# Performance work log

Measured on AMD Instinct MI355X. Metric: run time of the kernel, lower is better.

Reference implementation:

```python
import jax, jax.numpy as jnp
import numpy as np

TOP_K = 2
LORA_SCALE = 32.0 / 16.0  # alpha / r


def setup_inputs() -> dict:
    key = jax.random.key(0)
    ks = jax.random.split(key, 11)
    B, S, H, I, E, R = 4, 2048, 2048, 5504, 8, 16
    s = lambda k, shape, fan: jax.random.normal(k, shape, jnp.float32) / np.sqrt(fan)
    return {
        "x": jax.random.normal(ks[0], (B, S, H), jnp.float32),
        "gate_values": jax.random.normal(ks[1], (B, E), jnp.float32),
        "Wg": s(ks[2], (I, H), H),
        "Ag": s(ks[3], (E, H, R), H),
        "Bg": s(ks[4], (E, R, I), R),
        "Wu": s(ks[5], (I, H), H),
        "Au": s(ks[6], (E, H, R), H),
        "Bu": s(ks[7], (E, R, I), R),
        "Wd": s(ks[8], (H, I), I),
        "Ad": s(ks[9], (E, I, R), I),
        "Bd": s(ks[10], (E, R, H), R),
    }


def _top_k_binary_gates(gate_values, k):
    # set top-k entries per row to 1.0, others 0.0 (bsz, num_experts)
    _, idx = jax.lax.top_k(gate_values, k)
    b = jnp.zeros_like(gate_values)
    rows = jnp.arange(gate_values.shape[0])[:, None]
    return b.at[rows, idx].set(1.0)


def _adapter_linear(x, W, A, B, binary_gates):
    # base: (b,s,in) @ (out,in)^T -> (b,s,out)
    base = jnp.einsum("bsh,oh->bso", x, W)
    # per-expert LoRA: gate e * x @ A_e @ B_e, summed over selected experts
    u = jnp.einsum("bsh,ehr->bser", x, A)            # (b,s,E,r) low-rank
    delta = jnp.einsum("bser,ero,be->bso", u, B, binary_gates)
    return base + LORA_SCALE * delta


def reference(x, gate_values, Wg, Ag, Bg, Wu, Au, Bu, Wd, Ad, Bd):
    g = _top_k_binary_gates(gate_values, TOP_K)
    gate_out = _adapter_linear(x, Wg, Ag, Bg, g)
    up_out = _adapter_linear(x, Wu, Au, Bu, g)
    h = jax.nn.silu(gate_out) * up_out              # SwiGLU
    return _adapter_linear(h, Wd, Ad, Bd, g)
```

## Files before the change

### kernel.cpp

```cpp
#include <hip/hip_runtime.h>
#include <stdint.h>

typedef unsigned short u16;
typedef __bf16 bf16x8 __attribute__((ext_vector_type(8)));
typedef float f32x4 __attribute__((ext_vector_type(4)));

#define AS1 __attribute__((address_space(1)))
#define AS3 __attribute__((address_space(3)))

__device__ __forceinline__ void g2l16(const void* g, void* l) {
  __builtin_amdgcn_global_load_lds((AS1 void*)(void*)g, (AS3 void*)l, 16, 0, 0);
}

__device__ __forceinline__ u16 f2bf(float f) {
  union { float f; uint32_t u; } v; v.f = f;
  return (u16)((v.u + 0x7fffu + ((v.u >> 16) & 1u)) >> 16);
}
__device__ __forceinline__ float bf2f(u16 b) {
  union { uint32_t u; float f; } v; v.u = ((uint32_t)b) << 16;
  return v.f;
}

__global__ void k_top2(const float* __restrict__ gv, int* __restrict__ idx) {
  int b = threadIdx.x;
  if (b < 4) {
    const float* g = gv + b * 8;
    int i1 = 0; float v1 = g[0];
    for (int e = 1; e < 8; ++e) if (g[e] > v1) { v1 = g[e]; i1 = e; }
    int i2 = -1; float v2 = -3.0e38f;
    for (int e = 0; e < 8; ++e) if (e != i1 && g[e] > v2) { v2 = g[e]; i2 = e; }
    idx[2 * b] = i1; idx[2 * b + 1] = i2;
  }
}

__global__ void k_cast(const float* __restrict__ in, u16* __restrict__ out, int n4) {
  int i = blockIdx.x * 256 + threadIdx.x;
  if (i < n4) {
    float4 v = ((const float4*)in)[i];
    ushort4 o = make_ushort4(f2bf(v.x), f2bf(v.y), f2bf(v.z), f2bf(v.w));
    ((ushort4*)out)[i] = o;
  }
}

__global__ void k_aT(const float* __restrict__ A0, const float* __restrict__ A1,
                     const int* __restrict__ idx, u16* __restrict__ out,
                     int Kd, int jmax) {
  int t = blockIdx.x * 256 + threadIdx.x;
  if (t >= 4 * jmax * Kd) return;
  int h = t % Kd;
  int j = (t / Kd) % jmax;
  int b = t / (Kd * jmax);
  const float* src = (j >= 32) ? A1 : A0;
  int jj = j & 31;
  int e = idx[2 * b + ((jj >> 4) & 1)];
  int r = jj & 15;
  out[t] = f2bf(src[((size_t)e * Kd + h) * 16 + r]);
}

__global__ void k_bT(const float* __restrict__ Bsrc, const int* __restrict__ idx,
                     u16* __restrict__ out, int N) {
  int t = blockIdx.x * 256 + threadIdx.x;
  if (t < 4 * N * 32) {
    int j = t & 31;
    int n = (t >> 5) % N;
    int b = t / (N * 32);
    int e = (j & 16) ? idx[2 * b + 1] : idx[2 * b];
    int r = j & 15;
    out[t] = f2bf(Bsrc[((size_t)e * 16 + r) * N + n]);
  }
}

template <int N2>
__global__ __launch_bounds__(256) void k_skinny(
    const u16* __restrict__ A, const u16* __restrict__ BT,
    float* __restrict__ part, int M, int K, int total_iters, int iters_per_chunk) {
  __shared__ u16 sA[128 * 64];
  __shared__ u16 sB[N2 * 64];
  int nm = M >> 7;
  int bm = blockIdx.x % nm, chunk = blockIdx.x / nm;
  int m0 = bm << 7;
  int batch = m0 >> 11;
  int tid = threadIdx.x, lane = tid & 63, w = tid >> 6;
  int kb = chunk * iters_per_chunk;
  int ke = min(total_iters, kb + iters_per_chunk);

  const u16* Bb = BT + (size_t)batch * N2 * K;

  const u16* ga[4]; u16* la[4];
  #pragma unroll
  for (int t = 0; t < 4; ++t) {
    int cb = 4 * w + t;
    int q = cb * 64 + lane;
    int row = q >> 3;
    int c = (q & 7) ^ (row & 7);
    ga[t] = A + (size_t)(m0 + row) * K + (size_t)kb * 64 + c * 8;
    la[t] = sA + cb * 512;
  }
  constexpr int nB = N2 / 32;
  const u16* gb[nB]; u16* lb[nB];
  #pragma unroll
  for (int t = 0; t < nB; ++t) {
    int cb = nB * w + t;
    int q = cb * 64 + lane;
    int row = q >> 3;
    int c = (q & 7) ^ (row & 7);
    gb[t] = Bb + (size_t)row * K + (size_t)kb * 64 + c * 8;
    lb[t] = sB + cb * 512;
  }

  f32x4 acc[2][N2 / 16] = {};
  for (int kt = kb; kt < ke; ++kt) {
    #pragma unroll
    for (int t = 0; t < 4; ++t) { g2l16(ga[t], la[t]); ga[t] += 64; }
    #pragma unroll
    for (int t = 0; t < nB; ++t) { g2l16(gb[t], lb[t]); gb[t] += 64; }
    __syncthreads();
    #pragma unroll
    for (int ks = 0; ks < 2; ++ks) {
      int cb0 = ks * 4 + (lane >> 4);
      bf16x8 af[2], bfr[N2 / 16];
      #pragma unroll
      for (int mi = 0; mi < 2; ++mi) {
        int row = 32 * w + mi * 16 + (lane & 15);
        af[mi] = *(const bf16x8*)(sA + (row * 8 + (cb0 ^ (row & 7))) * 8);
      }
      #pragma unroll
      for (int ni = 0; ni < N2 / 16; ++ni) {
        int row = ni * 16 + (lane & 15);
        bfr[ni] = *(const bf16x8*)(sB + (row * 8 + (cb0 ^ (row & 7))) * 8);
      }
      #pragma unroll
      for (int mi = 0; mi < 2; ++mi)
        #pragma unroll
        for (int ni = 0; ni < N2 / 16; ++ni)
          acc[mi][ni] = __builtin_amdgcn_mfma_f32_16x16x32_bf16(
              af[mi], bfr[ni], acc[mi][ni], 0, 0, 0);
    }
    __syncthreads();
  }

  int rb = (lane >> 4) * 4, cc = lane & 15;
  #pragma unroll
  for (int mi = 0; mi < 2; ++mi)
    #pragma unroll
    for (int ni = 0; ni < N2 / 16; ++ni)
      #pragma unroll
      for (int reg = 0; reg < 4; ++reg) {
        int gr = m0 + 32 * w + mi * 16 + rb + reg;
        int gc = ni * 16 + cc;
        part[((size_t)chunk * M + gr) * N2 + gc] = acc[mi][ni][reg];
      }
}

__global__ void k_fin(const float* __restrict__ part, u16* __restrict__ out0,
                      u16* __restrict__ out1, int M, int N2, int nch) {
  int t = blockIdx.x * 256 + threadIdx.x;
  if (t >= M * N2) return;
  float s = 0.f;
  for (int c = 0; c < nch; ++c) s += part[(size_t)c * M * N2 + t];
  int j = t % N2, bs = t / N2;
  u16 v = f2bf(2.0f * s);
  if (N2 == 64) {
    if (j < 32) out0[(size_t)bs * 32 + j] = v;
    else        out1[(size_t)bs * 32 + (j - 32)] = v;
  } else {
    out0[(size_t)bs * 32 + j] = v;
  }
}

__global__ __launch_bounds__(256, 3)
void k_gemm(const u16* __restrict__ A, const u16* __restrict__ Bm,
            const u16* __restrict__ A2, const u16* __restrict__ B2,
            const u16* Gprev, void* Out,
            int N, int K, int mode) {
  __shared__ u16 sA[128 * 64];
  __shared__ u16 sB[128 * 64];
  int nt = N >> 7;
  int nm = gridDim.x / nt;
  int perx = nm >> 3;
  int xcd = blockIdx.x & 7;
  int v = blockIdx.x >> 3;
  int bn = v / perx;
  int bm = xcd * perx + (v - bn * perx);
  int m0 = bm << 7, n0 = bn << 7;
  int tid = threadIdx.x, lane = tid & 63, w = tid >> 6;
  int mo = (w & 1) << 6, no = (w >> 1) << 6;

  const u16* ga[4]; const u16* gb[4];
  u16* la[4]; u16* lb[4];
  #pragma unroll
  for (int t = 0; t < 4; ++t) {
    int cb = 4 * w + t;
    int q = cb * 64 + lane;
    int row = q >> 3;
    int c = (q & 7) ^ (row & 7);
    ga[t] = A + (size_t)(m0 + row) * K + c * 8;
    gb[t] = Bm + (size_t)(n0 + row) * K + c * 8;
    la[t] = sA + cb * 512;
    lb[t] = sB + cb * 512;
  }

  f32x4 acc[4][4] = {};

  int kiters = K >> 6;
  for (int kt = 0; kt < kiters; ++kt) {
    #pragma unroll
    for (int t = 0; t < 4; ++t) { g2l16(ga[t], la[t]); ga[t] += 64; }
    #pragma unroll
    for (int t = 0; t < 4; ++t) { g2l16(gb[t], lb[t]); gb[t] += 64; }
    __syncthreads();
    #pragma unroll
    for (int ks = 0; ks < 2; ++ks) {
      bf16x8 af[4], bfr[4];
      int cb0 = ks * 4 + (lane >> 4);
      #pragma unroll
      for (int mi = 0; mi < 4; ++mi) {
        int row = mo + mi * 16 + (lane & 15);
        af[mi] = *(const bf16x8*)(sA + (row * 8 + (cb0 ^ (row & 7))) * 8);
      }
      #pragma unroll
      for (int ni = 0; ni < 4; ++ni) {
        int row = no + ni * 16 + (lane & 15);
        bfr[ni] = *(const bf16x8*)(sB + (row * 8 + (cb0 ^ (row & 7))) * 8);
      }
      #pragma unroll
      for (int mi = 0; mi < 4; ++mi)
        #pragma unroll
        for (int ni = 0; ni < 4; ++ni)
          acc[mi][ni] = __builtin_amdgcn_mfma_f32_16x16x32_bf16(
              af[mi], bfr[ni], acc[mi][ni], 0, 0, 0);
    }
    __syncthreads();
  }

  {
    int batch = m0 >> 11;
    const u16* B2b = B2 + (size_t)batch * N * 32;
    #pragma unroll
    for (int t = 0; t < 2; ++t) {
      int cb = 2 * w + t;
      int q = cb * 64 + lane;
      int row = q >> 2;
      int c = (q & 3) ^ (row & 3);
      g2l16(A2 + (size_t)(m0 + row) * 32 + c * 8, sA + cb * 512);
      g2l16(B2b + (size_t)(n0 + row) * 32 + c * 8, sB + cb * 512);
    }
    __syncthreads();
    bf16x8 af[4], bfr[4];
    int c0 = lane >> 4;
    #pragma unroll
    for (int mi = 0; mi < 4; ++mi) {
      int row = mo + mi * 16 + (lane & 15);
      af[mi] = *(const bf16x8*)(sA + (row * 4 + (c0 ^ (row & 3))) * 8);
    }
    #pragma unroll
    for (int ni = 0; ni < 4; ++ni) {
      int row = no + ni * 16 + (lane & 15);
      bfr[ni] = *(const bf16x8*)(sB + (row * 4 + (c0 ^ (row & 3))) * 8);
    }
    #pragma unroll
    for (int mi = 0; mi < 4; ++mi)
      #pragma unroll
      for (int ni = 0; ni < 4; ++ni)
        acc[mi][ni] = __builtin_amdgcn_mfma_f32_16x16x32_bf16(
            af[mi], bfr[ni], acc[mi][ni], 0, 0, 0);
  }

  int rb = (lane >> 4) * 4;
  int cc = lane & 15;
  #pragma unroll
  for (int mi = 0; mi < 4; ++mi) {
    #pragma unroll
    for (int ni = 0; ni < 4; ++ni) {
      #pragma unroll
      for (int reg = 0; reg < 4; ++reg) {
        int gr = m0 + mo + mi * 16 + rb + reg;
        int gc = n0 + no + ni * 16 + cc;
        size_t pos = (size_t)gr * N + gc;
        float v = acc[mi][ni][reg];
        if (mode == 0) {
          v = v / (1.f + __expf(-v));
          ((u16*)Out)[pos] = f2bf(v);
        } else if (mode == 1) {
          float g = bf2f(Gprev[pos]);
          ((u16*)Out)[pos] = f2bf(g * v);
        } else {
          ((float*)Out)[pos] = v;
        }
      }
    }
  }
}

extern "C" void kernel_launch(void* const* d_in, const int* in_sizes, int n_in,
                              void* d_out, int out_size, void* d_ws, size_t ws_size,
                              hipStream_t stream) {
  const float* x  = (const float*)d_in[0];
  const float* gv = (const float*)d_in[1];
  const float* Wg = (const float*)d_in[2];
  const float* Ag = (const float*)d_in[3];
  const float* Bg = (const float*)d_in[4];
  const float* Wu = (const float*)d_in[5];
  const float* Au = (const float*)d_in[6];
  const float* Bu = (const float*)d_in[7];
  const float* Wd = (const float*)d_in[8];
  const float* Ad = (const float*)d_in[9];
  const float* Bd = (const float*)d_in[10];
  float* out = (float*)d_out;

  char* ws = (char*)d_ws;
  size_t off = 0;
  auto alloc = [&](size_t bytes) -> void* {
    void* p = ws + off;
    off = (off + bytes + 255) & ~(size_t)255;
    return p;
  };
  int* idx  = (int*)alloc(32);
  u16* xb   = (u16*)alloc((size_t)8192 * 2048 * 2);
  u16* Wgb  = (u16*)alloc((size_t)5504 * 2048 * 2);
  u16* Wub  = (u16*)alloc((size_t)5504 * 2048 * 2);
  u16* Wdb  = (u16*)alloc((size_t)2048 * 5504 * 2);
  u16* xag  = (u16*)alloc((size_t)8192 * 32 * 2);
  u16* xau  = (u16*)alloc((size_t)8192 * 32 * 2);
  u16* ha   = (u16*)alloc((size_t)8192 * 32 * 2);
  u16* BgT  = (u16*)alloc((size_t)4 * 5504 * 32 * 2);
  u16* BuT  = (u16*)alloc((size_t)4 * 5504 * 32 * 2);
  u16* BdT  = (u16*)alloc((size_t)4 * 2048 * 32 * 2);
  u16* AxT  = (u16*)alloc((size_t)4 * 64 * 2048 * 2);
  u16* AdT  = (u16*)alloc((size_t)4 * 32 * 5504 * 2);
  u16* gbuf = (u16*)alloc((size_t)8192 * 5504 * 2);
  if (off > ws_size) return;

  float* part_xa = (float*)gbuf;
  float* part_ha = (float*)Wgb;

  k_top2<<<1, 64, 0, stream>>>(gv, idx);
  k_cast<<<16384, 256, 0, stream>>>(x, xb, 4194304);
  k_cast<<<11008, 256, 0, stream>>>(Wg, Wgb, 2818048);
  k_cast<<<11008, 256, 0, stream>>>(Wu, Wub, 2818048);
  k_cast<<<11008, 256, 0, stream>>>(Wd, Wdb, 2818048);
  k_aT<<<2048, 256, 0, stream>>>(Ag, Au, idx, AxT, 2048, 64);
  k_aT<<<2752, 256, 0, stream>>>(Ad, Ad, idx, AdT, 5504, 32);
  k_bT<<<2752, 256, 0, stream>>>(Bg, idx, BgT, 5504);
  k_bT<<<2752, 256, 0, stream>>>(Bu, idx, BuT, 5504);
  k_bT<<<1024, 256, 0, stream>>>(Bd, idx, BdT, 2048);

  k_skinny<64><<<64 * 4, 256, 0, stream>>>(xb, AxT, part_xa, 8192, 2048, 32, 8);
  k_fin<<<2048, 256, 0, stream>>>(part_xa, xag, xau, 8192, 64, 4);

  k_gemm<<<64 * 43, 256, 0, stream>>>(xb, Wgb, xag, BgT, (const u16*)nullptr,
                                      gbuf, 5504, 2048, 0);
  k_gemm<<<64 * 43, 256, 0, stream>>>(xb, Wub, xau, BuT, gbuf, gbuf, 5504, 2048, 1);

  k_skinny<32><<<64 * 4, 256, 0, stream>>>(gbuf, AdT, part_ha, 8192, 5504, 86, 22);
  k_fin<<<1024, 256, 0, stream>>>(part_ha, ha, ha, 8192, 32, 4);

  k_gemm<<<64 * 16, 256, 0, stream>>>(gbuf, Wdb, ha, BdT, (const u16*)nullptr,
                                      out, 2048, 5504, 2);
}
```

Before: 880.8 us.

## Replace 128x128 GEMM with 256x256 double-buffered 8-wave GEMM and pad N

Swaps the 128x128 tile, 4-wave GEMM for a 256x256 tile, 512-thread kernel. The new kernel double-buffers LDS through a 128KB buffer, prefetches the next K tiles with direct global-to-LDS loads that interleave with MFMA quadrants, and uses explicit waitcnt, barrier and priority control. The intermediate dimension is padded from 5504 to 5632 so the 256-wide tiles divide evenly, with zero-padded weight casts and B transposes. The Wd cast now reuses the Wu buffer after the gate/up GEMMs. The aim is higher arithmetic intensity per tile and less load stall, at the cost of extra padded work, higher register/LDS pressure and lower occupancy.

```diff
diff --git a/kernel.cpp b/kernel.cpp
--- a/kernel.cpp
+++ b/kernel.cpp
@@ -20,6 +20,20 @@
   union { uint32_t u; float f; } v; v.u = ((uint32_t)b) << 16;
   return v.f;
 }
+
+__device__ __forceinline__ bf16x8 dsr(uint32_t a) {
+  bf16x8 r;
+  asm volatile("ds_read_b128 %0, %1" : "=v"(r) : "v"(a));
+  return r;
+}
+__device__ __forceinline__ void barx() {
+  __builtin_amdgcn_sched_barrier(0);
+  __builtin_amdgcn_s_barrier();
+  __builtin_amdgcn_sched_barrier(0);
+}
+#define LGKM0 do { asm volatile("s_waitcnt lgkmcnt(0)" ::: "memory"); \
+                   __builtin_amdgcn_sched_barrier(0); } while (0)
+#define VMCNT(n) asm volatile("s_waitcnt vmcnt(" #n ")" ::: "memory")
 
 __global__ void k_top2(const float* __restrict__ gv, int* __restrict__ idx) {
   int b = threadIdx.x;
@@ -40,6 +54,27 @@
     ushort4 o = make_ushort4(f2bf(v.x), f2bf(v.y), f2bf(v.z), f2bf(v.w));
     ((ushort4*)out)[i] = o;
   }
+}
+
+__global__ void k_cast2d(const float* __restrict__ in, u16* __restrict__ out,
+                         int Rs, int Cs, int total4, int Co) {
+  int i = blockIdx.x * 256 + threadIdx.x;
+  if (i >= total4) return;
+  size_t e0 = (size_t)i * 4;
+  int c = (int)(e0 % Co);
+  int r = (int)(e0 / Co);
+  ushort4 o;
+  if (r < Rs && c + 3 < Cs) {
+    float4 v = *(const float4*)(in + (size_t)r * Cs + c);
+    o = make_ushort4(f2bf(v.x), f2bf(v.y), f2bf(v.z), f2bf(v.w));
+  } else {
+    u16 a[4];
+    #pragma unroll
+    for (int k = 0; k < 4; ++k)
+      a[k] = (r < Rs && c + k < Cs) ? f2bf(in[(size_t)r * Cs + c + k]) : (u16)0;
+    o = make_ushort4(a[0], a[1], a[2], a[3]);
+  }
+  *(ushort4*)(out + e0) = o;
 }
 
 __global__ void k_aT(const float* __restrict__ A0, const float* __restrict__ A1,
@@ -58,22 +93,23 @@
 }
 
 __global__ void k_bT(const float* __restrict__ Bsrc, const int* __restrict__ idx,
-                     u16* __restrict__ out, int N) {
+                     u16* __restrict__ out, int Nout, int Nsrc) {
   int t = blockIdx.x * 256 + threadIdx.x;
-  if (t < 4 * N * 32) {
+  if (t < 4 * Nout * 32) {
     int j = t & 31;
-    int n = (t >> 5) % N;
-    int b = t / (N * 32);
+    int n = (t >> 5) % Nout;
+    int b = t / (Nout * 32);
     int e = (j & 16) ? idx[2 * b + 1] : idx[2 * b];
     int r = j & 15;
-    out[t] = f2bf(Bsrc[((size_t)e * 16 + r) * N + n]);
+    out[t] = (n < Nsrc) ? f2bf(Bsrc[((size_t)e * 16 + r) * Nsrc + n]) : (u16)0;
   }
 }
 
 template <int N2>
 __global__ __launch_bounds__(256) void k_skinny(
     const u16* __restrict__ A, const u16* __restrict__ BT,
-    float* __restrict__ part, int M, int K, int total_iters, int iters_per_chunk) {
+    float* __restrict__ part, int M, int lda, int K, int total_iters,
+    int iters_per_chunk) {
   __shared__ u16 sA[128 * 64];
   __shared__ u16 sB[N2 * 64];
   int nm = M >> 7;
@@ -93,7 +129,7 @@
     int q = cb * 64 + lane;
     int row = q >> 3;
     int c = (q & 7) ^ (row & 7);
-    ga[t] = A + (size_t)(m0 + row) * K + (size_t)kb * 64 + c * 8;
+    ga[t] = A + (size_t)(m0 + row) * lda + (size_t)kb * 64 + c * 8;
     la[t] = sA + cb * 512;
   }
   constexpr int nB = N2 / 32;
@@ -168,128 +204,188 @@
   }
 }
 
-__global__ __launch_bounds__(256, 3)
-void k_gemm(const u16* __restrict__ A, const u16* __restrict__ Bm,
-            const u16* __restrict__ A2, const u16* __restrict__ B2,
-            const u16* Gprev, void* Out,
-            int N, int K, int mode) {
-  __shared__ u16 sA[128 * 64];
-  __shared__ u16 sB[128 * 64];
-  int nt = N >> 7;
+__global__ __launch_bounds__(512, 2)
+void k_gemm256(const u16* __restrict__ A, const u16* __restrict__ Bm,
+               const u16* __restrict__ A2, const u16* __restrict__ B2,
+               const u16* __restrict__ Gprev, void* __restrict__ Out,
+               int N, int K, int mode) {
+  __shared__ u16 lds[65536];
+  int nt = N >> 8;
   int nm = gridDim.x / nt;
   int perx = nm >> 3;
   int xcd = blockIdx.x & 7;
   int v = blockIdx.x >> 3;
   int bn = v / perx;
   int bm = xcd * perx + (v - bn * perx);
-  int m0 = bm << 7, n0 = bn << 7;
-  int tid = threadIdx.x, lane = tid & 63, w = tid >> 6;
-  int mo = (w & 1) << 6, no = (w >> 1) << 6;
-
-  const u16* ga[4]; const u16* gb[4];
-  u16* la[4]; u16* lb[4];
-  #pragma unroll
-  for (int t = 0; t < 4; ++t) {
-    int cb = 4 * w + t;
-    int q = cb * 64 + lane;
-    int row = q >> 3;
-    int c = (q & 7) ^ (row & 7);
-    ga[t] = A + (size_t)(m0 + row) * K + c * 8;
-    gb[t] = Bm + (size_t)(n0 + row) * K + c * 8;
-    la[t] = sA + cb * 512;
-    lb[t] = sB + cb * 512;
-  }
-
-  f32x4 acc[4][4] = {};
+  int m0 = bm << 8, n0 = bn << 8;
+  int batch = m0 >> 11;
+
+  int tid = threadIdx.x;
+  int lane = tid & 63, w = tid >> 6;
+  int wm = w >> 2, wn = w & 3;
+  int g = lane >> 4, l7 = lane & 7, l15 = lane & 15;
+
+  int srow = w * 8 + (lane >> 3);
+  int scol = ((lane & 7) ^ (lane >> 3)) * 8;
+  const u16* pA = A + (size_t)(m0 + srow) * K + scol;
+  const u16* pB = Bm + (size_t)(n0 + srow) * K + scol;
+
+  uint32_t Lb = (uint32_t)(uint64_t)(&lds[0]);
+  uint32_t aTh0 = (uint32_t)(wm * 8192 + l15 * 128 + ((g ^ l7) * 16));
+  uint32_t aTh1 = aTh0 ^ 64;
+  uint32_t bTh0 = (uint32_t)(wn * 4096 + l15 * 128 + ((g ^ l7) * 16));
+  uint32_t bTh1 = bTh0 ^ 64;
+
+  f32x4 acc[2][4][2][2] = {};
+  bf16x8 af[4][2], bfr[2][2];
 
   int kiters = K >> 6;
-  for (int kt = 0; kt < kiters; ++kt) {
-    #pragma unroll
-    for (int t = 0; t < 4; ++t) { g2l16(ga[t], la[t]); ga[t] += 64; }
-    #pragma unroll
-    for (int t = 0; t < 4; ++t) { g2l16(gb[t], lb[t]); gb[t] += 64; }
-    __syncthreads();
-    #pragma unroll
-    for (int ks = 0; ks < 2; ++ks) {
-      bf16x8 af[4], bfr[4];
-      int cb0 = ks * 4 + (lane >> 4);
-      #pragma unroll
-      for (int mi = 0; mi < 4; ++mi) {
-        int row = mo + mi * 16 + (lane & 15);
-        af[mi] = *(const bf16x8*)(sA + (row * 8 + (cb0 ^ (row & 7))) * 8);
-      }
-      #pragma unroll
-      for (int ni = 0; ni < 4; ++ni) {
-        int row = no + ni * 16 + (lane & 15);
-        bfr[ni] = *(const bf16x8*)(sB + (row * 8 + (cb0 ^ (row & 7))) * 8);
-      }
+
+#define STAGE_A(h1, jt_) do { \
+    u16* _d = lds + (((jt_) & 1) << 14) + ((h1) * 8192) + (w << 9); \
+    const u16* _s = pA + (size_t)((h1) * 128) * K + (((size_t)(jt_)) << 6); \
+    g2l16(_s, _d); \
+    g2l16(_s + (size_t)64 * K, _d + 4096); \
+  } while (0)
+#define STAGE_B(h1, jt_) do { \
+    u16* _d = lds + 32768 + (((jt_) & 1) << 14) + ((h1) * 8192) + (w << 9); \
+    const u16* _s = pB + (size_t)((h1) * 128) * K + (((size_t)(jt_)) << 6); \
+    g2l16(_s, _d); \
+    g2l16(_s + (size_t)64 * K, _d + 4096); \
+  } while (0)
+#define LDA(mh, bufb) do { \
+    uint32_t _b = Lb + (bufb) + (mh) * 16384; \
+    _Pragma("unroll") for (int mi = 0; mi < 4; ++mi) { \
+      af[mi][0] = dsr(_b + aTh0 + mi * 2048); \
+      af[mi][1] = dsr(_b + aTh1 + mi * 2048); \
+    } } while (0)
+#define LDB(nh, bufb) do { \
+    uint32_t _b = Lb + 65536 + (bufb) + (nh) * 16384; \
+    _Pragma("unroll") for (int ni = 0; ni < 2; ++ni) { \
+      bfr[ni][0] = dsr(_b + bTh0 + ni * 2048); \
+      bfr[ni][1] = dsr(_b + bTh1 + ni * 2048); \
+    } } while (0)
+#define MFMA_Q(mh, nh) do { \
+    __builtin_amdgcn_s_setprio(1); \
+    _Pragma("unroll") for (int ks = 0; ks < 2; ++ks) \
+      _Pragma("unroll") for (int mi = 0; mi < 4; ++mi) \
+        _Pragma("unroll") for (int ni = 0; ni < 2; ++ni) \
+          acc[mh][mi][nh][ni] = __builtin_amdgcn_mfma_f32_16x16x32_bf16( \
+              af[mi][ks], bfr[ni][ks], acc[mh][mi][nh][ni], 0, 0, 0); \
+    __builtin_amdgcn_s_setprio(0); \
+  } while (0)
+
+  STAGE_A(0, 0); STAGE_A(1, 0); STAGE_B(0, 0); STAGE_B(1, 0);
+  STAGE_A(0, 1); STAGE_A(1, 1);
+  VMCNT(4);
+  barx();
+
+  int jt = 0;
+  for (; jt < kiters - 2; ++jt) {
+    uint32_t bufb = (uint32_t)((jt & 1) << 15);
+    LDA(0, bufb); LDB(0, bufb);
+    STAGE_B(0, jt + 1);
+    barx(); LGKM0; MFMA_Q(0, 0); barx();
+    LDB(1, bufb);
+    STAGE_B(1, jt + 1);
+    barx(); LGKM0; MFMA_Q(0, 1); barx();
+    LDA(1, bufb);
+    STAGE_A(0, jt + 2);
+    barx(); LGKM0; MFMA_Q(1, 1); barx();
+    LDB(0, bufb);
+    STAGE_A(1, jt + 2);
+    VMCNT(4);
+    barx(); LGKM0; MFMA_Q(1, 0); barx();
+  }
+  {
+    uint32_t bufb = (uint32_t)((jt & 1) << 15);
+    LDA(0, bufb); LDB(0, bufb);
+    STAGE_B(0, kiters - 1);
+    barx(); LGKM0; MFMA_Q(0, 0); barx();
+    LDB(1, bufb);
+    STAGE_B(1, kiters - 1);
+    barx(); LGKM0; MFMA_Q(0, 1); barx();
+    LDA(1, bufb);
+    barx(); LGKM0; MFMA_Q(1, 1); barx();
+    LDB(0, bufb);
+    VMCNT(0);
+    barx(); LGKM0; MFMA_Q(1, 0); barx();
+  }
+  {
+    uint32_t bufb = (uint32_t)(((kiters - 1) & 1) << 15);
+    LDA(0, bufb); LDB(0, bufb); LGKM0; MFMA_Q(0, 0);
+    LDB(1, bufb); LGKM0; MFMA_Q(0, 1);
+    LDA(1, bufb); LGKM0; MFMA_Q(1, 1);
+    LDB(0, bufb); LGKM0; MFMA_Q(1, 0);
+  }
+
+  {
+    const u16* B2b = B2 + (size_t)batch * N * 32;
+    int srow2 = w * 16 + (lane >> 2);
+    int scol2 = ((lane & 3) ^ ((lane >> 2) & 3)) * 8;
+    const u16* pA2 = A2 + (size_t)(m0 + srow2) * 32 + scol2;
+    const u16* pB2 = B2b + (size_t)(n0 + srow2) * 32 + scol2;
+    barx();
+    {
+      u16* dA = lds + (w << 9);
+      g2l16(pA2, dA); g2l16(pA2 + 4096, dA + 4096);
+      u16* dB = lds + 32768 + (w << 9);
+      g2l16(pB2, dB); g2l16(pB2 + 4096, dB + 4096);
+    }
+    VMCNT(0);
+    barx();
+    uint32_t c2 = (uint32_t)((g ^ (lane & 3)) * 16);
+    bf16x8 af2[4], bf2[2];
+    #pragma unroll
+    for (int mh = 0; mh < 2; ++mh) {
       #pragma unroll
       for (int mi = 0; mi < 4; ++mi)
+        af2[mi] = dsr(Lb + mh * 8192 + wm * 4096 + mi * 1024 + l15 * 64 + c2);
+      #pragma unroll
+      for (int nh = 0; nh < 2; ++nh) {
+        bf2[0] = dsr(Lb + 65536 + nh * 8192 + wn * 2048 + l15 * 64 + c2);
+        bf2[1] = dsr(Lb + 65536 + nh * 8192 + wn * 2048 + 1024 + l15 * 64 + c2);
+        LGKM0;
         #pragma unroll
-        for (int ni = 0; ni < 4; ++ni)
-          acc[mi][ni] = __builtin_amdgcn_mfma_f32_16x16x32_bf16(
-              af[mi], bfr[ni], acc[mi][ni], 0, 0, 0);
-    }
-    __syncthreads();
-  }
-
-  {
-    int batch = m0 >> 11;
-    const u16* B2b = B2 + (size_t)batch * N * 32;
-    #pragma unroll
-    for (int t = 0; t < 2; ++t) {
-      int cb = 2 * w + t;
-      int q = cb * 64 + lane;
-      int row = q >> 2;
-      int c = (q & 3) ^ (row & 3);
-      g2l16(A2 + (size_t)(m0 + row) * 32 + c * 8, sA + cb * 512);
-      g2l16(B2b + (size_t)(n0 + row) * 32 + c * 8, sB + cb * 512);
-    }
-    __syncthreads();
-    bf16x8 af[4], bfr[4];
-    int c0 = lane >> 4;
-    #pragma unroll
-    for (int mi = 0; mi < 4; ++mi) {
-      int row = mo + mi * 16 + (lane & 15);
-      af[mi] = *(const bf16x8*)(sA + (row * 4 + (c0 ^ (row & 3))) * 8);
-    }
-    #pragma unroll
-    for (int ni = 0; ni < 4; ++ni) {
-      int row = no + ni * 16 + (lane & 15);
-      bfr[ni] = *(const bf16x8*)(sB + (row * 4 + (c0 ^ (row & 3))) * 8);
-    }
-    #pragma unroll
-    for (int mi = 0; mi < 4; ++mi)
-      #pragma unroll
-      for (int ni = 0; ni < 4; ++ni)
-        acc[mi][ni] = __builtin_amdgcn_mfma_f32_16x16x32_bf16(
-            af[mi], bfr[ni], acc[mi][ni], 0, 0, 0);
-  }
-
-  int rb = (lane >> 4) * 4;
-  int cc = lane & 15;
-  #pragma unroll
-  for (int mi = 0; mi < 4; ++mi) {
-    #pragma unroll
-    for (int ni = 0; ni < 4; ++ni) {
-      #pragma unroll
-      for (int reg = 0; reg < 4; ++reg) {
-        int gr = m0 + mo + mi * 16 + rb + reg;
-        int gc = n0 + no + ni * 16 + cc;
-        size_t pos = (size_t)gr * N + gc;
-        float v = acc[mi][ni][reg];
-        if (mode == 0) {
-          v = v / (1.f + __expf(-v));
-          ((u16*)Out)[pos] = f2bf(v);
-        } else if (mode == 1) {
-          float g = bf2f(Gprev[pos]);
-          ((u16*)Out)[pos] = f2bf(g * v);
-        } else {
-          ((float*)Out)[pos] = v;
-        }
+        for (int mi = 0; mi < 4; ++mi)
+          #pragma unroll
+          for (int ni = 0; ni < 2; ++ni)
+            acc[mh][mi][nh][ni] = __builtin_amdgcn_mfma_f32_16x16x32_bf16(
+                af2[mi], bf2[ni], acc[mh][mi][nh][ni], 0, 0, 0);
       }
     }
   }
+
+  int rb = (lane >> 4) * 4, cc = lane & 15;
+  #pragma unroll
+  for (int mh = 0; mh < 2; ++mh)
+    #pragma unroll
+    for (int mi = 0; mi < 4; ++mi)
+      #pragma unroll
+      for (int nh = 0; nh < 2; ++nh)
+        #pragma unroll
+        for (int ni = 0; ni < 2; ++ni)
+          #pragma unroll
+          for (int reg = 0; reg < 4; ++reg) {
+            int gr = m0 + mh * 128 + wm * 64 + mi * 16 + rb + reg;
+            int gc = n0 + nh * 128 + wn * 32 + ni * 16 + cc;
+            size_t pos = (size_t)gr * N + gc;
+            float vv = acc[mh][mi][nh][ni][reg];
+            if (mode == 0) {
+              vv = vv / (1.f + __expf(-vv));
+              ((u16*)Out)[pos] = f2bf(vv);
+            } else if (mode == 1) {
+              float gg = bf2f(Gprev[pos]);
+              ((u16*)Out)[pos] = f2bf(gg * vv);
+            } else {
+              ((float*)Out)[pos] = vv;
+            }
+          }
+#undef STAGE_A
+#undef STAGE_B
+#undef LDA
+#undef LDB
+#undef MFMA_Q
 }
 
 extern "C" void kernel_launch(void* const* d_in, const int* in_sizes, int n_in,
@@ -317,44 +413,46 @@
   };
   int* idx  = (int*)alloc(32);
   u16* xb   = (u16*)alloc((size_t)8192 * 2048 * 2);
-  u16* Wgb  = (u16*)alloc((size_t)5504 * 2048 * 2);
-  u16* Wub  = (u16*)alloc((size_t)5504 * 2048 * 2);
-  u16* Wdb  = (u16*)alloc((size_t)2048 * 5504 * 2);
+  u16* Wgb  = (u16*)alloc((size_t)5632 * 2048 * 2);
+  u16* Wub  = (u16*)alloc((size_t)5632 * 2048 * 2);
   u16* xag  = (u16*)alloc((size_t)8192 * 32 * 2);
   u16* xau  = (u16*)alloc((size_t)8192 * 32 * 2);
   u16* ha   = (u16*)alloc((size_t)8192 * 32 * 2);
-  u16* BgT  = (u16*)alloc((size_t)4 * 5504 * 32 * 2);
-  u16* BuT  = (u16*)alloc((size_t)4 * 5504 * 32 * 2);
+  u16* BgT  = (u16*)alloc((size_t)4 * 5632 * 32 * 2);
+  u16* BuT  = (u16*)alloc((size_t)4 * 5632 * 32 * 2);
   u16* BdT  = (u16*)alloc((size_t)4 * 2048 * 32 * 2);
   u16* AxT  = (u16*)alloc((size_t)4 * 64 * 2048 * 2);
   u16* AdT  = (u16*)alloc((size_t)4 * 32 * 5504 * 2);
-  u16* gbuf = (u16*)alloc((size_t)8192 * 5504 * 2);
+  u16* gbuf = (u16*)alloc((size_t)8192 * 5632 * 2);
   if (off > ws_size) return;
 
+  u16* Wdb = Wub;
   float* part_xa = (float*)gbuf;
   float* part_ha = (float*)Wgb;
 
   k_top2<<<1, 64, 0, stream>>>(gv, idx);
   k_cast<<<16384, 256, 0, stream>>>(x, xb, 4194304);
-  k_cast<<<11008, 256, 0, stream>>>(Wg, Wgb, 2818048);
-  k_cast<<<11008, 256, 0, stream>>>(Wu, Wub, 2818048);
-  k_cast<<<11008, 256, 0, stream>>>(Wd, Wdb, 2818048);
+  k_cast2d<<<11264, 256, 0, stream>>>(Wg, Wgb, 5504, 2048, 2883584, 2048);
+  k_cast2d<<<11264, 256, 0, stream>>>(Wu, Wub, 5504, 2048, 2883584, 2048);
   k_aT<<<2048, 256, 0, stream>>>(Ag, Au, idx, AxT, 2048, 64);
   k_aT<<<2752, 256, 0, stream>>>(Ad, Ad, idx, AdT, 5504, 32);
-  k_bT<<<2752, 256, 0, stream>>>(Bg, idx, BgT, 5504);
-  k_bT<<<2752, 256, 0, stream>>>(Bu, idx, BuT, 5504);
-  k_bT<<<1024, 256, 0, stream>>>(Bd, idx, BdT, 2048);
-
-  k_skinny<64><<<64 * 4, 256, 0, stream>>>(xb, AxT, part_xa, 8192, 2048, 32, 8);
+  k_bT<<<2816, 256, 0, stream>>>(Bg, idx, BgT, 5632, 5504);
+  k_bT<<<2816, 256, 0, stream>>>(Bu, idx, BuT, 5632, 5504);
+  k_bT<<<1024, 256, 0, stream>>>(Bd, idx, BdT, 2048, 2048);
+
+  k_skinny<64><<<64 * 4, 256, 0, stream>>>(xb, AxT, part_xa, 8192, 2048, 2048, 32, 8);
   k_fin<<<2048, 256, 0, stream>>>(part_xa, xag, xau, 8192, 64, 4);
 
-  k_gemm<<<64 * 43, 256, 0, stream>>>(xb, Wgb, xag, BgT, (const u16*)nullptr,
-                                      gbuf, 5504, 2048, 0);
-  k_gemm<<<64 * 43, 256, 0, stream>>>(xb, Wub, xau, BuT, gbuf, gbuf, 5504, 2048, 1);
-
-  k_skinny<32><<<64 * 4, 256, 0, stream>>>(gbuf, AdT, part_ha, 8192, 5504, 86, 22);
+  k_gemm256<<<32 * 22, 512, 0, stream>>>(xb, Wgb, xag, BgT, (const u16*)nullptr,
+                                         gbuf, 5632, 2048, 0);
+  k_gemm256<<<32 * 22, 512, 0, stream>>>(xb, Wub, xau, BuT, gbuf,
+                                         gbuf, 5632, 2048, 1);
+
+  k_cast2d<<<11264, 256, 0, stream>>>(Wd, Wdb, 2048, 5504, 2883584, 5632);
+
+  k_skinny<32><<<64 * 4, 256, 0, stream>>>(gbuf, AdT, part_ha, 8192, 5632, 5504, 86, 22);
   k_fin<<<1024, 256, 0, stream>>>(part_ha, ha, ha, 8192, 32, 4);
 
-  k_gemm<<<64 * 16, 256, 0, stream>>>(gbuf, Wdb, ha, BdT, (const u16*)nullptr,
-                                      out, 2048, 5504, 2);
-}
+  k_gemm256<<<32 * 8, 512, 0, stream>>>(gbuf, Wdb, ha, BdT, (const u16*)nullptr,
+                                        out, 2048, 5632, 2);
+}
```

After: 912.6 us. +3.6%, slower.

## Fuse gate and up projection GEMMs into one kernel sharing the A tile

Applied to the files above, without the earlier changes.

Replaces the two separate gate and up GEMM launches with a single kernel that loads each x tile once and multiplies it against both the Wg and Wu tiles, keeping two accumulator sets. SiLU(gate)*up is applied directly in the epilogue. This removes the second read of x, the write and re-read of the intermediate gate buffer, and one launch. In exchange it doubles accumulator registers and raises LDS use to three tiles, so occupancy drops to 2 blocks per CU.

```diff
diff --git a/kernel.cpp b/kernel.cpp
--- a/kernel.cpp
+++ b/kernel.cpp
@@ -165,6 +165,143 @@
     else        out1[(size_t)bs * 32 + (j - 32)] = v;
   } else {
     out0[(size_t)bs * 32 + j] = v;
+  }
+}
+
+__global__ __launch_bounds__(256, 2)
+void k_gemmGU(const u16* __restrict__ A, const u16* __restrict__ Bg_,
+              const u16* __restrict__ Bu_,
+              const u16* __restrict__ A2g, const u16* __restrict__ A2u,
+              const u16* __restrict__ B2g, const u16* __restrict__ B2u,
+              u16* __restrict__ Out, int N, int K) {
+  __shared__ u16 sA[128 * 64];
+  __shared__ u16 sG[128 * 64];
+  __shared__ u16 sU[128 * 64];
+  int nt = N >> 7;
+  int nm = gridDim.x / nt;
+  int perx = nm >> 3;
+  int xcd = blockIdx.x & 7;
+  int v = blockIdx.x >> 3;
+  int bn = v / perx;
+  int bm = xcd * perx + (v - bn * perx);
+  int m0 = bm << 7, n0 = bn << 7;
+  int tid = threadIdx.x, lane = tid & 63, w = tid >> 6;
+  int mo = (w & 1) << 6, no = (w >> 1) << 6;
+
+  const u16* ga[4]; const u16* gg[4]; const u16* gu[4];
+  u16* la[4]; u16* lg[4]; u16* lu[4];
+  #pragma unroll
+  for (int t = 0; t < 4; ++t) {
+    int cb = 4 * w + t;
+    int q = cb * 64 + lane;
+    int row = q >> 3;
+    int c = (q & 7) ^ (row & 7);
+    ga[t] = A + (size_t)(m0 + row) * K + c * 8;
+    gg[t] = Bg_ + (size_t)(n0 + row) * K + c * 8;
+    gu[t] = Bu_ + (size_t)(n0 + row) * K + c * 8;
+    la[t] = sA + cb * 512;
+    lg[t] = sG + cb * 512;
+    lu[t] = sU + cb * 512;
+  }
+
+  f32x4 accg[4][4] = {};
+  f32x4 accu[4][4] = {};
+
+  int kiters = K >> 6;
+  for (int kt = 0; kt < kiters; ++kt) {
+    #pragma unroll
+    for (int t = 0; t < 4; ++t) { g2l16(ga[t], la[t]); ga[t] += 64; }
+    #pragma unroll
+    for (int t = 0; t < 4; ++t) { g2l16(gg[t], lg[t]); gg[t] += 64; }
+    #pragma unroll
+    for (int t = 0; t < 4; ++t) { g2l16(gu[t], lu[t]); gu[t] += 64; }
+    __syncthreads();
+    #pragma unroll
+    for (int ks = 0; ks < 2; ++ks) {
+      bf16x8 af[4], bgf[4], buf_[4];
+      int cb0 = ks * 4 + (lane >> 4);
+      #pragma unroll
+      for (int mi = 0; mi < 4; ++mi) {
+        int row = mo + mi * 16 + (lane & 15);
+        af[mi] = *(const bf16x8*)(sA + (row * 8 + (cb0 ^ (row & 7))) * 8);
+      }
+      #pragma unroll
+      for (int ni = 0; ni < 4; ++ni) {
+        int row = no + ni * 16 + (lane & 15);
+        bgf[ni] = *(const bf16x8*)(sG + (row * 8 + (cb0 ^ (row & 7))) * 8);
+        buf_[ni] = *(const bf16x8*)(sU + (row * 8 + (cb0 ^ (row & 7))) * 8);
+      }
+      #pragma unroll
+      for (int mi = 0; mi < 4; ++mi)
+        #pragma unroll
+        for (int ni = 0; ni < 4; ++ni) {
+          accg[mi][ni] = __builtin_amdgcn_mfma_f32_16x16x32_bf16(
+              af[mi], bgf[ni], accg[mi][ni], 0, 0, 0);
+          accu[mi][ni] = __builtin_amdgcn_mfma_f32_16x16x32_bf16(
+              af[mi], buf_[ni], accu[mi][ni], 0, 0, 0);
+        }
+    }
+    __syncthreads();
+  }
+
+  {
+    int batch = m0 >> 11;
+    const u16* B2gb = B2g + (size_t)batch * N * 32;
+    const u16* B2ub = B2u + (size_t)batch * N * 32;
+    #pragma unroll
+    for (int t = 0; t < 2; ++t) {
+      int cb = 2 * w + t;
+      int q = cb * 64 + lane;
+      int row = q >> 2;
+      int c = (q & 3) ^ (row & 3);
+      g2l16(A2g + (size_t)(m0 + row) * 32 + c * 8, sA + cb * 512);
+      g2l16(A2u + (size_t)(m0 + row) * 32 + c * 8, sA + 4096 + cb * 512);
+      g2l16(B2gb + (size_t)(n0 + row) * 32 + c * 8, sG + cb * 512);
+      g2l16(B2ub + (size_t)(n0 + row) * 32 + c * 8, sU + cb * 512);
+    }
+    __syncthreads();
+    int c0 = lane >> 4;
+    bf16x8 ag2[4], au2[4], bg2[4], bu2[4];
+    #pragma unroll
+    for (int mi = 0; mi < 4; ++mi) {
+      int row = mo + mi * 16 + (lane & 15);
+      ag2[mi] = *(const bf16x8*)(sA + (row * 4 + (c0 ^ (row & 3))) * 8);
+      au2[mi] = *(const bf16x8*)(sA + 4096 + (row * 4 + (c0 ^ (row & 3))) * 8);
+    }
+    #pragma unroll
+    for (int ni = 0; ni < 4; ++ni) {
+      int row = no + ni * 16 + (lane & 15);
+      bg2[ni] = *(const bf16x8*)(sG + (row * 4 + (c0 ^ (row & 3))) * 8);
+      bu2[ni] = *(const bf16x8*)(sU + (row * 4 + (c0 ^ (row & 3))) * 8);
+    }
+    #pragma unroll
+    for (int mi = 0; mi < 4; ++mi)
+      #pragma unroll
+      for (int ni = 0; ni < 4; ++ni) {
+        accg[mi][ni] = __builtin_amdgcn_mfma_f32_16x16x32_bf16(
+            ag2[mi], bg2[ni], accg[mi][ni], 0, 0, 0);
+        accu[mi][ni] = __builtin_amdgcn_mfma_f32_16x16x32_bf16(
+            au2[mi], bu2[ni], accu[mi][ni], 0, 0, 0);
+      }
+  }
+
+  int rb = (lane >> 4) * 4;
+  int cc = lane & 15;
+  #pragma unroll
+  for (int mi = 0; mi < 4; ++mi) {
+    #pragma unroll
+    for (int ni = 0; ni < 4; ++ni) {
+      #pragma unroll
+      for (int reg = 0; reg < 4; ++reg) {
+        int gr = m0 + mo + mi * 16 + rb + reg;
+        int gc = n0 + no + ni * 16 + cc;
+        size_t pos = (size_t)gr * N + gc;
+        float gvv = accg[mi][ni][reg];
+        float uvv = accu[mi][ni][reg];
+        gvv = gvv / (1.f + __expf(-gvv));
+        Out[pos] = f2bf(gvv * uvv);
+      }
+    }
   }
 }
 
@@ -277,15 +414,15 @@
         int gr = m0 + mo + mi * 16 + rb + reg;
         int gc = n0 + no + ni * 16 + cc;
         size_t pos = (size_t)gr * N + gc;
-        float v = acc[mi][ni][reg];
+        float vv = acc[mi][ni][reg];
         if (mode == 0) {
-          v = v / (1.f + __expf(-v));
-          ((u16*)Out)[pos] = f2bf(v);
+          vv = vv / (1.f + __expf(-vv));
+          ((u16*)Out)[pos] = f2bf(vv);
         } else if (mode == 1) {
-          float g = bf2f(Gprev[pos]);
-          ((u16*)Out)[pos] = f2bf(g * v);
+          float gg = bf2f(Gprev[pos]);
+          ((u16*)Out)[pos] = f2bf(gg * vv);
         } else {
-          ((float*)Out)[pos] = v;
+          ((float*)Out)[pos] = vv;
         }
       }
     }
@@ -348,9 +485,8 @@
   k_skinny<64><<<64 * 4, 256, 0, stream>>>(xb, AxT, part_xa, 8192, 2048, 32, 8);
   k_fin<<<2048, 256, 0, stream>>>(part_xa, xag, xau, 8192, 64, 4);
 
-  k_gemm<<<64 * 43, 256, 0, stream>>>(xb, Wgb, xag, BgT, (const u16*)nullptr,
-                                      gbuf, 5504, 2048, 0);
-  k_gemm<<<64 * 43, 256, 0, stream>>>(xb, Wub, xau, BuT, gbuf, gbuf, 5504, 2048, 1);
+  k_gemmGU<<<64 * 43, 256, 0, stream>>>(xb, Wgb, Wub, xag, xau, BgT, BuT,
+                                        gbuf, 5504, 2048);
 
   k_skinny<32><<<64 * 4, 256, 0, stream>>>(gbuf, AdT, part_ha, 8192, 5504, 86, 22);
   k_fin<<<1024, 256, 0, stream>>>(part_ha, ha, ha, 8192, 32, 4);
```

New measurement: 818.5 us. -7.1%, faster.
